# Kernel tuning notes

Hardware: AMD Instinct MI355X
Metric: run time of the kernel (lower is better)

The kernel has to match this reference:

```python
import jax, jax.numpy as jnp
import numpy as np

N, E, G, M = 65536, 262144, 1024, 64   # nodes, edges, graphs, max nodes/graph
D, H, C, ED, P, L = 512, 8, 64, 128, 1024, 5  # hidden, heads, head_dim, edge_dim, proj_dim, layers
SLOPE = 0.2  # PyG GATv2 leaky_relu negative slope


def rmsnorm(x, w):
    eps = jnp.asarray(jnp.finfo(x.dtype).eps, x.dtype)
    return x * jax.lax.rsqrt(jnp.mean(x * x, axis=-1, keepdims=True) + eps) * w


def gat_layer(x, src, dst, eattr, Wl, bl, Wr, br, We, att, gb):
    # GATv2Conv(concat=True, edge_dim, add_self_loops=False), eval mode
    xl = (x @ Wl + bl).reshape(N, H, C)
    xr = (x @ Wr + br).reshape(N, H, C)
    ee = (eattr @ We).reshape(E, H, C)
    s = xl[src] + xr[dst] + ee                      # [E,H,C]
    s = jnp.where(s > 0, s, SLOPE * s)              # leaky_relu
    logits = jnp.einsum('ehc,hc->eh', s, att)       # [E,H]
    mx = jax.ops.segment_max(logits, dst, num_segments=N)
    p = jnp.exp(logits - mx[dst])
    denom = jax.ops.segment_sum(p, dst, num_segments=N)
    alpha = p / denom[dst]                          # segment softmax over in-edges of dst
    msg = xl[src] * alpha[:, :, None]               # [E,H,C]
    return jax.ops.segment_sum(msg, dst, num_segments=N).reshape(N, H * C) + gb


def setup_inputs():
    key = jax.random.key(0)
    ks = jax.random.split(key, 32)
    f = lambda k, shp: 0.02 * jax.random.normal(k, shp, dtype=jnp.float32)
    inp = {}
    inp['node_x'] = jax.random.randint(ks[0], (N, 9), 0, 2, dtype=jnp.int32)
    inp['edge_attr_idx'] = jax.random.randint(ks[1], (E, 3), 0, 2, dtype=jnp.int32)
    inp['edge_index'] = jax.random.randint(ks[2], (2, E), 0, N, dtype=jnp.int32)
    inp['batch'] = jnp.arange(N, dtype=jnp.int32) // M  # sorted graph ids, 64 atoms/graph
    # MolEncoder embedding tables, padded to max vocab (indices stay in-range)
    inp['atom_emb'] = f(ks[3], (9, 119, D))
    inp['edge_emb'] = f(ks[4], (3, 22, ED))
    # 5 GATv2Block layers, params stacked on leading axis
    inp['Wl'] = f(ks[5], (L, D, D)); inp['bl'] = f(ks[6], (L, D))
    inp['Wr'] = f(ks[7], (L, D, D)); inp['br'] = f(ks[8], (L, D))
    inp['We'] = f(ks[9], (L, ED, D))
    inp['att'] = f(ks[10], (L, H, C))
    inp['gb'] = f(ks[11], (L, D))
    inp['n1w'] = jnp.ones((L, D), jnp.float32)
    inp['f1w'] = f(ks[12], (L, D, 4 * D)); inp['f1b'] = f(ks[13], (L, 4 * D))
    inp['f2w'] = f(ks[14], (L, 4 * D, D)); inp['f2b'] = f(ks[15], (L, D))
    inp['n2w'] = jnp.ones((L, D), jnp.float32)
    # attention pooling + projection head
    inp['gapW'] = f(ks[16], (D, D)); inp['gapb'] = f(ks[17], (D,))
    inp['avW'] = f(ks[18], (D,)); inp['avb'] = f(ks[19], (1,))
    inp['p1W'] = f(ks[20], (D, P)); inp['p1b'] = f(ks[21], (P,))
    inp['pnw'] = jnp.ones((P,), jnp.float32)
    inp['p2W'] = f(ks[22], (P, P)); inp['p2b'] = f(ks[23], (P,))
    return inp


def reference(node_x, edge_attr_idx, edge_index, batch, atom_emb, edge_emb, Wl, bl, Wr, br, We, att, gb, n1w, f1w, f1b, f2w, f2b, n2w, gapW, gapb, avW, avb, p1W, p1b, pnw, p2W, p2b):
    src, dst = edge_index[0], edge_index[1]
    # MolEncoder: sum of categorical embeddings
    x = atom_emb[jnp.arange(9)[None, :], node_x].sum(axis=1)              # [N,D]
    eattr = edge_emb[jnp.arange(3)[None, :], edge_attr_idx].sum(axis=1)   # [E,ED]
    for l in range(L):
        xa = gat_layer(x, src, dst, eattr, Wl[l], bl[l], Wr[l], br[l], We[l], att[l], gb[l])
        x = rmsnorm(x + xa, n1w[l])
        h = jax.nn.gelu(x @ f1w[l] + f1b[l], approximate=False) @ f2w[l] + f2b[l]
        x = rmsnorm(x + h, n2w[l])
    # to_dense_batch with static max_nodes = M
    counts = jax.ops.segment_sum(jnp.ones(N, jnp.int32), batch, num_segments=G)
    starts = jnp.concatenate([jnp.zeros(1, jnp.int32), jnp.cumsum(counts)[:-1].astype(jnp.int32)])
    pos = jnp.arange(N, dtype=jnp.int32) - starts[batch]
    x_dense = jnp.zeros((G, M, D), x.dtype).at[batch, pos].set(x)
    mask = jnp.zeros((G, M), bool).at[batch, pos].set(True)
    # graph attention pooling
    z = x_dense @ gapW + gapb                                             # [G,M,D]
    a = (z @ avW + avb[0])[:, :, None]                                    # [G,M,1]
    a = jnp.where(mask[:, :, None], a, -jnp.inf)
    alpha = jax.nn.softmax(a, axis=1)
    h_graph = jnp.sum(z * alpha, axis=1)                                  # [G,D]
    hp = jax.nn.relu(rmsnorm(h_graph @ p1W + p1b, pnw))
    z_graph_pool = hp @ p2W + p2b                                         # [G,P]
    return z_graph_pool, x_dense, mask
```

## Files before the change

### kernel.cpp

```cpp
#include <hip/hip_runtime.h>
#include <hip/hip_bf16.h>
#include <math.h>

namespace {

using bf16 = __hip_bfloat16;
typedef __bf16 bf16x8 __attribute__((ext_vector_type(8)));
typedef float f32x4 __attribute__((ext_vector_type(4)));

constexpr int N_ = 65536, E_ = 262144, G_ = 1024, M_ = 64;
constexpr int D_ = 512, H_ = 8, C_ = 64, ED_ = 128, P_ = 1024, L_ = 5;
constexpr float SLOPE = 0.2f;
constexpr float EPSF = 1.1920929e-7f;

constexpr int NCH = 2;
constexpr int NCHUNK = N_ / NCH;

constexpr int TV = 22;
constexpr int TK = TV * TV * TV;
constexpr int TKP = 10752;

constexpr int CH = 4;

__device__ inline float b2f(bf16 h) { return __bfloat162float(h); }
__device__ inline bf16 f2b(float f) { return __float2bfloat16(f); }
__device__ inline float us2f(unsigned short u) {
  return __uint_as_float((unsigned)u << 16);
}
__device__ inline unsigned short f2us(float f) {
  bf16 b = __float2bfloat16(f);
  return *(unsigned short*)&b;
}

typedef __attribute__((address_space(1))) void as1_void_t;
typedef __attribute__((address_space(3))) void as3_void_t;
__device__ inline void gload16(const void* g, void* l) {
  __builtin_amdgcn_global_load_lds((const as1_void_t*)g, (as3_void_t*)l, 16, 0,
                                   0);
}

template <int EPI, int OBF>
__global__ __launch_bounds__(256) void mfma_gemm_k(
    const ushort* __restrict__ A, const ushort* __restrict__ Bt,
    const float* __restrict__ bias, void* __restrict__ Cv, int M, int K,
    int Nc) {
  __shared__ __align__(16) ushort As[128 * 64];
  __shared__ __align__(16) ushort Bs[128 * 64];
  const int tid = threadIdx.x;
  const int wave = tid >> 6, lane = tid & 63;
  const int m0 = blockIdx.x * 128, n0 = blockIdx.y * 128;
  const int wr = wave >> 1, wc = wave & 1;
  const int srow = tid >> 3;
  const int skoff = (((tid & 7) ^ (srow & 7)) << 3);
  const ushort* Ap = A + (size_t)(m0 + srow) * K + skoff;
  const ushort* Bp = Bt + (size_t)(n0 + srow) * K + skoff;
  char* AsB = (char*)As + wave * 1024;
  char* BsB = (char*)Bs + wave * 1024;
  const int fr = lane & 15, fg = lane >> 4;
  const int rx = fr & 7;
  const int sA0 = ((fg) ^ rx) << 3;
  const int sA1 = ((4 | fg) ^ rx) << 3;
  const ushort* Arow = As + (wr * 64 + fr) * 64;
  const ushort* Brow = Bs + (wc * 64 + fr) * 64;
  f32x4 acc[4][4];
#pragma unroll
  for (int i = 0; i < 4; ++i)
#pragma unroll
    for (int j = 0; j < 4; ++j) acc[i][j] = (f32x4){0.f, 0.f, 0.f, 0.f};

  for (int kt = 0; kt < K; kt += 64) {
#pragma unroll
    for (int r = 0; r < 4; ++r) {
      gload16(Ap + kt + (size_t)r * 32 * K, AsB + r * 4096);
      gload16(Bp + kt + (size_t)r * 32 * K, BsB + r * 4096);
    }
    __syncthreads();
    bf16x8 af[4], bg[4];
#pragma unroll
    for (int i = 0; i < 4; ++i)
      af[i] = *(const bf16x8*)(Arow + i * 1024 + sA0);
#pragma unroll
    for (int j = 0; j < 4; ++j)
      bg[j] = *(const bf16x8*)(Brow + j * 1024 + sA0);
#pragma unroll
    for (int i = 0; i < 4; ++i)
#pragma unroll
      for (int j = 0; j < 4; ++j)
        acc[i][j] = __builtin_amdgcn_mfma_f32_16x16x32_bf16(af[i], bg[j],
                                                            acc[i][j], 0, 0, 0);
#pragma unroll
    for (int i = 0; i < 4; ++i)
      af[i] = *(const bf16x8*)(Arow + i * 1024 + sA1);
#pragma unroll
    for (int j = 0; j < 4; ++j)
      bg[j] = *(const bf16x8*)(Brow + j * 1024 + sA1);
#pragma unroll
    for (int i = 0; i < 4; ++i)
#pragma unroll
      for (int j = 0; j < 4; ++j)
        acc[i][j] = __builtin_amdgcn_mfma_f32_16x16x32_bf16(af[i], bg[j],
                                                            acc[i][j], 0, 0, 0);
    __syncthreads();
  }
  const int cb = n0 + wc * 64 + fr;
  float bv[4];
#pragma unroll
  for (int j = 0; j < 4; ++j) bv[j] = bias ? bias[cb + j * 16] : 0.f;
#pragma unroll
  for (int i = 0; i < 4; ++i) {
#pragma unroll
    for (int r = 0; r < 4; ++r) {
      int m = m0 + wr * 64 + i * 16 + fg * 4 + r;
      size_t rb = (size_t)m * Nc + cb;
#pragma unroll
      for (int j = 0; j < 4; ++j) {
        float c = acc[i][j][r] + bv[j];
        if (EPI == 1) c = 0.5f * c * (1.f + erff(c * 0.70710678118654752f));
        if (OBF)
          ((bf16*)Cv)[rb + j * 16] = f2b(c);
        else
          ((float*)Cv)[rb + j * 16] = c;
      }
    }
  }
}

__global__ __launch_bounds__(256) void transpose_cvt_k(
    const float* __restrict__ W, bf16* __restrict__ Wt, int K, int N) {
  __shared__ float tile[32][33];
  int bn = blockIdx.x * 32, bk = blockIdx.y * 32;
  int tx = threadIdx.x, ty = threadIdx.y;
#pragma unroll
  for (int i = ty; i < 32; i += 8) tile[i][tx] = W[(size_t)(bk + i) * N + bn + tx];
  __syncthreads();
#pragma unroll
  for (int i = ty; i < 32; i += 8)
    Wt[(size_t)(bn + i) * K + bk + tx] = f2b(tile[tx][i]);
}

template <int EPI, typename TIN, typename TOUT>
__global__ __launch_bounds__(256) void gemm_bias_k(
    const TIN* __restrict__ A, const float* __restrict__ B,
    const float* __restrict__ bias, TOUT* __restrict__ C, int M, int K,
    int Nc) {
  __shared__ float As[64][17];
  __shared__ float Bs[16][68];
  const int tid = threadIdx.x;
  const int m0 = blockIdx.x * 64;
  const int n0 = blockIdx.y * 64;
  const int ty = tid >> 4, tx = tid & 15;
  const int lam = tid >> 2;
  const int lak = (tid & 3) << 2;
  const int lbk = tid >> 4;
  const int lbn = (tid & 15) << 2;
  const TIN* Aptr = A + (long)(m0 + lam) * K + lak;
  const float* Bptr = B + (long)lbk * Nc + n0 + lbn;
  float acc[4][4] = {};
  for (int kt = 0; kt < K; kt += 16) {
    float4 va = *(const float4*)(Aptr + kt);
    float4 vb = *(const float4*)(Bptr + (long)kt * Nc);
    __syncthreads();
    As[lam][lak + 0] = va.x; As[lam][lak + 1] = va.y;
    As[lam][lak + 2] = va.z; As[lam][lak + 3] = va.w;
    Bs[lbk][lbn + 0] = vb.x; Bs[lbk][lbn + 1] = vb.y;
    Bs[lbk][lbn + 2] = vb.z; Bs[lbk][lbn + 3] = vb.w;
    __syncthreads();
#pragma unroll
    for (int kk = 0; kk < 16; ++kk) {
      float a[4], b[4];
#pragma unroll
      for (int i = 0; i < 4; ++i) a[i] = As[ty * 4 + i][kk];
#pragma unroll
      for (int j = 0; j < 4; ++j) b[j] = Bs[kk][tx * 4 + j];
#pragma unroll
      for (int i = 0; i < 4; ++i)
#pragma unroll
        for (int j = 0; j < 4; ++j) acc[i][j] = fmaf(a[i], b[j], acc[i][j]);
    }
  }
#pragma unroll
  for (int i = 0; i < 4; ++i) {
    long row = (long)(m0 + ty * 4 + i) * Nc + n0;
#pragma unroll
    for (int j = 0; j < 4; ++j) {
      float c = acc[i][j] + (bias ? bias[n0 + tx * 4 + j] : 0.f);
      if (EPI == 1) c = 0.5f * c * (1.f + erff(c * 0.70710678118654752f));
      ((float*)C)[row + tx * 4 + j] = c;
    }
  }
}

__global__ __launch_bounds__(256) void encode_nodes_k(
    const int* __restrict__ nodeX, const float* __restrict__ atomEmb,
    bf16* __restrict__ x) {
  int n = blockIdx.x, tid = threadIdx.x;
  __shared__ int idx[9];
  if (tid < 9) idx[tid] = nodeX[n * 9 + tid];
  __syncthreads();
  for (int d = tid; d < D_; d += 256) {
    float s = 0.f;
#pragma unroll
    for (int k = 0; k < 9; ++k) s += atomEmb[(k * 119 + idx[k]) * D_ + d];
    x[(long)n * D_ + d] = f2b(s);
  }
}

__global__ __launch_bounds__(256) void build_keys_k(
    const int* __restrict__ eai, int* __restrict__ keys) {
  int e = blockIdx.x * 256 + threadIdx.x;
  keys[e] = eai[e * 3] * (TV * TV) + eai[e * 3 + 1] * TV + eai[e * 3 + 2];
}

__global__ __launch_bounds__(128) void build_eattr_tab_k(
    const float* __restrict__ edgeEmb, bf16* __restrict__ tab) {
  int r = blockIdx.x, d = threadIdx.x;
  float s = 0.f;
  if (r < TK) {
    int k0 = r / (TV * TV), k1 = (r / TV) % TV, k2 = r % TV;
    s = edgeEmb[(0 * TV + k0) * ED_ + d] + edgeEmb[(1 * TV + k1) * ED_ + d] +
        edgeEmb[(2 * TV + k2) * ED_ + d];
  }
  tab[(size_t)r * ED_ + d] = f2b(s);
}

__global__ __launch_bounds__(256) void gat_fused_k(
    bf16* __restrict__ x, const ushort* __restrict__ xl,
    const ushort* __restrict__ xr, const ushort* __restrict__ ee_tab,
    const int* __restrict__ keys, const float* __restrict__ att,
    const int* __restrict__ ptr, const int* __restrict__ eid,
    const int* __restrict__ src, const float* __restrict__ gb,
    const float* __restrict__ w) {
  const int wave = threadIdx.x >> 6, lane = threadIdx.x & 63;
  const int n = blockIdx.x * 4 + wave;
  const int d0 = lane * 8;
  const int beg = ptr[n], deg = ptr[n + 1] - beg;

  float4 a0 = *(const float4*)(att + d0);
  float4 a1 = *(const float4*)(att + d0 + 4);
  float attv[8] = {a0.x, a0.y, a0.z, a0.w, a1.x, a1.y, a1.z, a1.w};
  uint4 xru = *(const uint4*)(xr + (size_t)n * D_ + d0);
  float xrf[8];
#pragma unroll
  for (int q = 0; q < 4; ++q) {
    unsigned u = (&xru.x)[q];
    xrf[2 * q] = us2f((ushort)u);
    xrf[2 * q + 1] = us2f((ushort)(u >> 16));
  }

  float m = -__builtin_inff(), den = 0.f;
  float acc[8] = {0.f, 0.f, 0.f, 0.f, 0.f, 0.f, 0.f, 0.f};

  for (int c0 = 0; c0 < deg; c0 += CH) {
    int cn = min(deg - c0, CH);
    int s_l = 0, k_l = 0;
    if (lane < cn) {
      int e = eid[beg + c0 + lane];
      s_l = src[e];
      k_l = keys[e];
    }
    uint4 xlv[CH];
    float lg[CH];
#pragma unroll
    for (int i = 0; i < CH; ++i) {
      lg[i] = -__builtin_inff();
      if (i < cn) {
        int s = __shfl(s_l, i);
        int k = __shfl(k_l, i);
        xlv[i] = *(const uint4*)(xl + (size_t)s * D_ + d0);
        uint4 ev = *(const uint4*)(ee_tab + (size_t)k * D_ + d0);
        float part = 0.f;
#pragma unroll
        for (int q = 0; q < 4; ++q) {
          unsigned ua = (&xlv[i].x)[q];
          unsigned ue = (&ev.x)[q];
          float v0 = us2f((ushort)ua) + xrf[2 * q] + us2f((ushort)ue);
          float v1 =
              us2f((ushort)(ua >> 16)) + xrf[2 * q + 1] + us2f((ushort)(ue >> 16));
          v0 = (v0 > 0.f) ? v0 : SLOPE * v0;
          v1 = (v1 > 0.f) ? v1 : SLOPE * v1;
          part = fmaf(v0, attv[2 * q], part);
          part = fmaf(v1, attv[2 * q + 1], part);
        }
        part += __shfl_xor(part, 1);
        part += __shfl_xor(part, 2);
        part += __shfl_xor(part, 4);
        lg[i] = part;
      }
    }
    float cm = lg[0];
#pragma unroll
    for (int i = 1; i < CH; ++i) cm = fmaxf(cm, lg[i]);
    if (cm > m) {
      float sc = expf(m - cm);
      den *= sc;
#pragma unroll
      for (int j = 0; j < 8; ++j) acc[j] *= sc;
      m = cm;
    }
#pragma unroll
    for (int i = 0; i < CH; ++i) {
      if (i < cn) {
        float p = expf(lg[i] - m);
        den += p;
#pragma unroll
        for (int q = 0; q < 4; ++q) {
          unsigned ua = (&xlv[i].x)[q];
          acc[2 * q] = fmaf(us2f((ushort)ua), p, acc[2 * q]);
          acc[2 * q + 1] = fmaf(us2f((ushort)(ua >> 16)), p, acc[2 * q + 1]);
        }
      }
    }
  }

  float inv = (deg > 0) ? 1.f / den : 0.f;
  uint4 xu = *(const uint4*)((const ushort*)x + (size_t)n * D_ + d0);
  float4 g0 = *(const float4*)(gb + d0);
  float4 g1 = *(const float4*)(gb + d0 + 4);
  float gbv[8] = {g0.x, g0.y, g0.z, g0.w, g1.x, g1.y, g1.z, g1.w};
  float v[8], ss = 0.f;
#pragma unroll
  for (int q = 0; q < 4; ++q) {
    unsigned u = (&xu.x)[q];
    v[2 * q] = us2f((ushort)u) + acc[2 * q] * inv + gbv[2 * q];
    v[2 * q + 1] = us2f((ushort)(u >> 16)) + acc[2 * q + 1] * inv + gbv[2 * q + 1];
  }
#pragma unroll
  for (int j = 0; j < 8; ++j) ss += v[j] * v[j];
#pragma unroll
  for (int o = 1; o < 64; o <<= 1) ss += __shfl_xor(ss, o);
  float scale = rsqrtf(ss * (1.0f / D_) + EPSF);
  float4 w0 = *(const float4*)(w + d0);
  float4 w1 = *(const float4*)(w + d0 + 4);
  float wv[8] = {w0.x, w0.y, w0.z, w0.w, w1.x, w1.y, w1.z, w1.w};
  uint4 outv;
#pragma unroll
  for (int q = 0; q < 4; ++q) {
    unsigned lo = f2us(v[2 * q] * scale * wv[2 * q]);
    unsigned hi = f2us(v[2 * q + 1] * scale * wv[2 * q + 1]);
    (&outv.x)[q] = lo | (hi << 16);
  }
  *(uint4*)((ushort*)x + (size_t)n * D_ + d0) = outv;
}

__global__ __launch_bounds__(256) void rmsnorm_res_k(
    bf16* __restrict__ x, const float* __restrict__ xa,
    const float* __restrict__ w) {
  int n = blockIdx.x, tid = threadIdx.x;
  long base = (long)n * D_;
  float v0 = b2f(x[base + tid]) + xa[base + tid];
  float v1 = b2f(x[base + tid + 256]) + xa[base + tid + 256];
  float ss = v0 * v0 + v1 * v1;
#pragma unroll
  for (int o = 32; o > 0; o >>= 1) ss += __shfl_xor(ss, o);
  __shared__ float wsum[4];
  if ((tid & 63) == 0) wsum[tid >> 6] = ss;
  __syncthreads();
  float tot = wsum[0] + wsum[1] + wsum[2] + wsum[3];
  float scale = rsqrtf(tot * (1.0f / D_) + EPSF);
  x[base + tid] = f2b(v0 * scale * w[tid]);
  x[base + tid + 256] = f2b(v1 * scale * w[tid + 256]);
}

__global__ void zero_int_k(int* __restrict__ p) {
  p[blockIdx.x * 256 + threadIdx.x] = 0;
}
__global__ void count_k(const int* __restrict__ key, int* __restrict__ counts) {
  int id = blockIdx.x * 256 + threadIdx.x;
  atomicAdd(&counts[key[id]], 1);
}
__global__ void copy_int_k(const int* __restrict__ in, int* __restrict__ out) {
  int id = blockIdx.x * 256 + threadIdx.x;
  out[id] = in[id];
}
__global__ void fill_csr_k(const int* __restrict__ dst,
                           int* __restrict__ cursor, int* __restrict__ eid) {
  int e = blockIdx.x * 256 + threadIdx.x;
  int pos = atomicAdd(&cursor[dst[e]], 1);
  eid[pos] = e;
}
__global__ __launch_bounds__(1024) void scanN_k(const int* __restrict__ cnt,
                                                int* __restrict__ ptr) {
  __shared__ int sums[1024];
  int t = threadIdx.x;
  int base = t * 64;
  int s = 0;
  for (int i = 0; i < 64; ++i) s += cnt[base + i];
  sums[t] = s;
  __syncthreads();
  for (int off = 1; off < 1024; off <<= 1) {
    int v = (t >= off) ? sums[t - off] : 0;
    __syncthreads();
    sums[t] += v;
    __syncthreads();
  }
  int run = (t > 0) ? sums[t - 1] : 0;
  for (int i = 0; i < 64; ++i) {
    ptr[base + i] = run;
    run += cnt[base + i];
  }
  if (t == 1023) ptr[N_] = run;
}
__global__ void scan_k(const int* __restrict__ counts, int* __restrict__ starts) {
  __shared__ int buf[G_];
  int t = threadIdx.x;
  int c = counts[t];
  buf[t] = c;
  __syncthreads();
  for (int off = 1; off < G_; off <<= 1) {
    int v = (t >= off) ? buf[t - off] : 0;
    __syncthreads();
    buf[t] += v;
    __syncthreads();
  }
  starts[t] = buf[t] - c;
}

__global__ __launch_bounds__(256) void pool_k(
    const bf16* __restrict__ z, const float* __restrict__ avW,
    const float* __restrict__ avb, const int* __restrict__ counts,
    const int* __restrict__ starts, float* __restrict__ hg) {
  int g = blockIdx.x, tid = threadIdx.x;
  int cnt = counts[g], st = starts[g];
  __shared__ float aL[M_];
  int wave = tid >> 6, lane = tid & 63;
  for (int m = wave; m < M_; m += 4) {
    float s = 0.f;
    if (m < cnt) {
      const bf16* row = z + (long)(st + m) * D_;
      for (int c = lane; c < D_; c += 64) s += b2f(row[c]) * avW[c];
    }
#pragma unroll
    for (int o = 32; o > 0; o >>= 1) s += __shfl_xor(s, o);
    if (lane == 0) aL[m] = s;
  }
  __syncthreads();
  if (tid < 64) {
    float v = (tid < cnt) ? aL[tid] + avb[0] : -__builtin_inff();
    float mxv = v;
#pragma unroll
    for (int o = 32; o > 0; o >>= 1) mxv = fmaxf(mxv, __shfl_xor(mxv, o));
    float p = (tid < cnt) ? expf(v - mxv) : 0.f;
    float sm = p;
#pragma unroll
    for (int o = 32; o > 0; o >>= 1) sm += __shfl_xor(sm, o);
    aL[tid] = p / sm;
  }
  __syncthreads();
  for (int d = tid; d < D_; d += 256) {
    float acc = 0.f;
    for (int m = 0; m < cnt; ++m) acc += b2f(z[(long)(st + m) * D_ + d]) * aL[m];
    hg[(long)g * D_ + d] = acc;
  }
}

__global__ __launch_bounds__(256) void rms_relu_k(
    const float* __restrict__ in, const float* __restrict__ w,
    float* __restrict__ out) {
  int g = blockIdx.x, tid = threadIdx.x;
  long base = (long)g * P_;
  float v[4], ss = 0.f;
#pragma unroll
  for (int k = 0; k < 4; ++k) {
    v[k] = in[base + tid + k * 256];
    ss += v[k] * v[k];
  }
#pragma unroll
  for (int o = 32; o > 0; o >>= 1) ss += __shfl_xor(ss, o);
  __shared__ float wsum[4];
  if ((tid & 63) == 0) wsum[tid >> 6] = ss;
  __syncthreads();
  float tot = wsum[0] + wsum[1] + wsum[2] + wsum[3];
  float scale = rsqrtf(tot * (1.0f / P_) + EPSF);
#pragma unroll
  for (int k = 0; k < 4; ++k) {
    float c = v[k] * scale * w[tid + k * 256];
    out[base + tid + k * 256] = fmaxf(c, 0.f);
  }
}

__global__ __launch_bounds__(256) void write_dense_k(
    const bf16* __restrict__ x, const int* __restrict__ counts,
    const int* __restrict__ starts, float* __restrict__ out1) {
  long id = (long)blockIdx.x * 256 + threadIdx.x;
  int g = (int)(id >> 15);
  int rem = (int)(id & 32767);
  int m = rem >> 9, d = rem & 511;
  float v = 0.f;
  if (m < counts[g]) v = b2f(x[(long)(starts[g] + m) * D_ + d]);
  out1[id] = v;
}
__global__ void write_mask_k(const int* __restrict__ counts,
                             float* __restrict__ out2) {
  int id = blockIdx.x * 256 + threadIdx.x;
  out2[id] = ((id & 63) < counts[id >> 6]) ? 1.f : 0.f;
}

}

extern "C" void kernel_launch(void* const* d_in, const int* in_sizes, int n_in,
                              void* d_out, int out_size, void* d_ws,
                              size_t ws_size, hipStream_t stream) {
  const int* node_x = (const int*)d_in[0];
  const int* edge_attr_idx = (const int*)d_in[1];
  const int* edge_index = (const int*)d_in[2];
  const int* batch = (const int*)d_in[3];
  const float* atom_emb = (const float*)d_in[4];
  const float* edge_emb = (const float*)d_in[5];
  const float* Wl = (const float*)d_in[6];
  const float* bl = (const float*)d_in[7];
  const float* Wr = (const float*)d_in[8];
  const float* br = (const float*)d_in[9];
  const float* We = (const float*)d_in[10];
  const float* att = (const float*)d_in[11];
  const float* gb = (const float*)d_in[12];
  const float* n1w = (const float*)d_in[13];
  const float* f1w = (const float*)d_in[14];
  const float* f1b = (const float*)d_in[15];
  const float* f2w = (const float*)d_in[16];
  const float* f2b = (const float*)d_in[17];
  const float* n2w = (const float*)d_in[18];
  const float* gapW = (const float*)d_in[19];
  const float* gapb = (const float*)d_in[20];
  const float* avW = (const float*)d_in[21];
  const float* avb = (const float*)d_in[22];
  const float* p1W = (const float*)d_in[23];
  const float* p1b = (const float*)d_in[24];
  const float* pnw = (const float*)d_in[25];
  const float* p2W = (const float*)d_in[26];
  const float* p2b = (const float*)d_in[27];
  const int* src = edge_index;
  const int* dst = edge_index + E_;

  char* ws = (char*)d_ws;
  bf16* x = (bf16*)ws;
  bf16* xl = x + (long)N_ * D_;
  bf16* xr = xl + (long)N_ * D_;
  bf16* region = xr + (long)N_ * D_;
  bf16* ee_tab = region;
  bf16* eattr_tab = ee_tab + (long)TKP * D_;
  float* logits_unused = (float*)(region + (long)32768 * D_ + (long)32768 * ED_);
  int* keys = (int*)(logits_unused + (long)E_ * H_);
  float* denom_unused = (float*)(keys + N_ * H_);
  int* counts = (int*)(denom_unused + (long)N_ * H_);
  int* starts = counts + G_;
  float* hg = (float*)(starts + G_);
  float* tmpP = hg + (long)G_ * D_;
  float* hp = tmpP + (long)G_ * P_;
  bf16* hid = xl;

  bf16* wsc = (bf16*)tmpP;
  bf16* Wl_b = wsc;
  bf16* Wr_b = Wl_b + 512 * 512;
  bf16* We_b = Wr_b + 512 * 512;
  bf16* f1w_b = We_b + 512 * 128;
  bf16* f2w_b = f1w_b + 2048 * 512;

  float* out0 = (float*)d_out;
  float* out1 = out0 + (long)G_ * P_;
  float* out2 = out1 + (long)G_ * M_ * D_;
  float* xa = out1;

  int* csr_eid = (int*)out0;
  int* csr_ptr = csr_eid + E_;
  int* cursor = csr_ptr + N_ + 1;

  encode_nodes_k<<<N_, 256, 0, stream>>>(node_x, atom_emb, x);

  build_keys_k<<<E_ / 256, 256, 0, stream>>>(edge_attr_idx, keys);
  build_eattr_tab_k<<<TKP, 128, 0, stream>>>(edge_emb, eattr_tab);
  zero_int_k<<<N_ / 256, 256, 0, stream>>>(cursor);
  count_k<<<E_ / 256, 256, 0, stream>>>(dst, cursor);
  scanN_k<<<1, 1024, 0, stream>>>(cursor, csr_ptr);
  copy_int_k<<<N_ / 256, 256, 0, stream>>>(csr_ptr, cursor);
  fill_csr_k<<<E_ / 256, 256, 0, stream>>>(dst, cursor, csr_eid);

  for (int l = 0; l < L_; ++l) {
    const float* Wl_l = Wl + (long)l * D_ * D_;
    const float* bl_l = bl + (long)l * D_;
    const float* Wr_l = Wr + (long)l * D_ * D_;
    const float* br_l = br + (long)l * D_;
    const float* We_l = We + (long)l * ED_ * D_;
    const float* att_l = att + (long)l * H_ * C_;
    const float* gb_l = gb + (long)l * D_;
    const float* n1w_l = n1w + (long)l * D_;
    const float* f1w_l = f1w + (long)l * D_ * 4 * D_;
    const float* f1b_l = f1b + (long)l * 4 * D_;
    const float* f2w_l = f2w + (long)l * 4 * D_ * D_;
    const float* f2b_l = f2b + (long)l * D_;
    const float* n2w_l = n2w + (long)l * D_;

    transpose_cvt_k<<<dim3(16, 16), dim3(32, 8), 0, stream>>>(Wl_l, Wl_b, 512, 512);
    transpose_cvt_k<<<dim3(16, 16), dim3(32, 8), 0, stream>>>(Wr_l, Wr_b, 512, 512);
    transpose_cvt_k<<<dim3(16, 4), dim3(32, 8), 0, stream>>>(We_l, We_b, 128, 512);
    transpose_cvt_k<<<dim3(64, 16), dim3(32, 8), 0, stream>>>(f1w_l, f1w_b, 512, 2048);
    transpose_cvt_k<<<dim3(16, 64), dim3(32, 8), 0, stream>>>(f2w_l, f2w_b, 2048, 512);

    mfma_gemm_k<0, 1><<<dim3(N_ / 128, D_ / 128), 256, 0, stream>>>(
        (const ushort*)x, (const ushort*)Wl_b, bl_l, xl, N_, D_, D_);
    mfma_gemm_k<0, 1><<<dim3(N_ / 128, D_ / 128), 256, 0, stream>>>(
        (const ushort*)x, (const ushort*)Wr_b, br_l, xr, N_, D_, D_);
    mfma_gemm_k<0, 1><<<dim3(TKP / 128, D_ / 128), 256, 0, stream>>>(
        (const ushort*)eattr_tab, (const ushort*)We_b, nullptr, ee_tab, TKP,
        ED_, D_);

    gat_fused_k<<<N_ / 4, 256, 0, stream>>>(
        x, (const ushort*)xl, (const ushort*)xr, (const ushort*)ee_tab, keys,
        att_l, csr_ptr, csr_eid, src, gb_l, n1w_l);

    for (int nc = 0; nc < NCH; ++nc) {
      long nbase = (long)nc * NCHUNK;
      mfma_gemm_k<1, 1><<<dim3(NCHUNK / 128, (4 * D_) / 128), 256, 0, stream>>>(
          (const ushort*)(x + nbase * D_), (const ushort*)f1w_b, f1b_l, hid,
          NCHUNK, D_, 4 * D_);
      mfma_gemm_k<0, 0><<<dim3(NCHUNK / 128, D_ / 128), 256, 0, stream>>>(
          (const ushort*)hid, (const ushort*)f2w_b, f2b_l, xa + nbase * D_,
          NCHUNK, 4 * D_, D_);
    }
    rmsnorm_res_k<<<N_, 256, 0, stream>>>(x, xa, n2w_l);
  }

  zero_int_k<<<G_ / 256, 256, 0, stream>>>(counts);
  count_k<<<N_ / 256, 256, 0, stream>>>(batch, counts);
  scan_k<<<1, G_, 0, stream>>>(counts, starts);

  bf16* gapW_b = eattr_tab;
  transpose_cvt_k<<<dim3(16, 16), dim3(32, 8), 0, stream>>>(gapW, gapW_b, 512, 512);
  mfma_gemm_k<0, 1><<<dim3(N_ / 128, D_ / 128), 256, 0, stream>>>(
      (const ushort*)x, (const ushort*)gapW_b, gapb, xl, N_, D_, D_);
  pool_k<<<G_, 256, 0, stream>>>(xl, avW, avb, counts, starts, hg);
  gemm_bias_k<0, float, float><<<dim3(G_ / 64, P_ / 64), 256, 0, stream>>>(
      hg, p1W, p1b, tmpP, G_, D_, P_);
  rms_relu_k<<<G_, 256, 0, stream>>>(tmpP, pnw, hp);
  gemm_bias_k<0, float, float><<<dim3(G_ / 64, P_ / 64), 256, 0, stream>>>(
      hp, p2W, p2b, out0, G_, P_, P_);

  write_dense_k<<<(int)(((long)G_ * M_ * D_) / 256), 256, 0, stream>>>(
      x, counts, starts, out1);
  write_mask_k<<<(G_ * M_) / 256, 256, 0, stream>>>(counts, out2);
}
```

Before: 4.118 ms.

## Double-buffer MFMA GEMM LDS, fuse Wl/Wr GEMMs, batch weight prep, fast GELU

The MFMA GEMM now uses two LDS buffers, so the next K tile's global-to-LDS loads are issued before the current tile is computed, which hides load latency and removes one barrier per iteration. The Wl and Wr projections are merged into a single N=1024 GEMM writing an interleaved xlr buffer, and the GAT kernel reads from it. The five per-layer weight transposes are merged into one prep kernel that also concatenates the two biases. erff in the GELU epilogue is replaced by an Abramowitz-Stegun polynomial approximation, which slightly changes numerics. Double buffering doubles LDS use to 64KB per block, which may lower occupancy.

```diff
diff --git a/kernel.cpp b/kernel.cpp
--- a/kernel.cpp
+++ b/kernel.cpp
@@ -30,6 +30,20 @@
 __device__ inline unsigned short f2us(float f) {
   bf16 b = __float2bfloat16(f);
   return *(unsigned short*)&b;
+}
+
+__device__ inline float fast_gelu(float c) {
+  float z = c * 0.70710678118654752f;
+  float az = fabsf(z);
+  float t = __builtin_amdgcn_rcpf(1.f + 0.3275911f * az);
+  float e = __expf(-az * az);
+  float poly =
+      t * (0.254829592f +
+           t * (-0.284496736f +
+                t * (1.421413741f + t * (-1.453152027f + t * 1.061405429f))));
+  float r = 1.f - poly * e;
+  float erfv = (z < 0.f) ? -r : r;
+  return 0.5f * c * (1.f + erfv);
 }
 
 typedef __attribute__((address_space(1))) void as1_void_t;
@@ -44,8 +58,8 @@
     const ushort* __restrict__ A, const ushort* __restrict__ Bt,
     const float* __restrict__ bias, void* __restrict__ Cv, int M, int K,
     int Nc) {
-  __shared__ __align__(16) ushort As[128 * 64];
-  __shared__ __align__(16) ushort Bs[128 * 64];
+  __shared__ __align__(16) ushort As[2][128 * 64];
+  __shared__ __align__(16) ushort Bs[2][128 * 64];
   const int tid = threadIdx.x;
   const int wave = tid >> 6, lane = tid & 63;
   const int m0 = blockIdx.x * 128, n0 = blockIdx.y * 128;
@@ -54,34 +68,33 @@
   const int skoff = (((tid & 7) ^ (srow & 7)) << 3);
   const ushort* Ap = A + (size_t)(m0 + srow) * K + skoff;
   const ushort* Bp = Bt + (size_t)(n0 + srow) * K + skoff;
-  char* AsB = (char*)As + wave * 1024;
-  char* BsB = (char*)Bs + wave * 1024;
   const int fr = lane & 15, fg = lane >> 4;
   const int rx = fr & 7;
   const int sA0 = ((fg) ^ rx) << 3;
   const int sA1 = ((4 | fg) ^ rx) << 3;
-  const ushort* Arow = As + (wr * 64 + fr) * 64;
-  const ushort* Brow = Bs + (wc * 64 + fr) * 64;
   f32x4 acc[4][4];
 #pragma unroll
   for (int i = 0; i < 4; ++i)
 #pragma unroll
     for (int j = 0; j < 4; ++j) acc[i][j] = (f32x4){0.f, 0.f, 0.f, 0.f};
 
-  for (int kt = 0; kt < K; kt += 64) {
+  auto STAGE = [&](int buf, int kt) {
 #pragma unroll
     for (int r = 0; r < 4; ++r) {
-      gload16(Ap + kt + (size_t)r * 32 * K, AsB + r * 4096);
-      gload16(Bp + kt + (size_t)r * 32 * K, BsB + r * 4096);
-    }
-    __syncthreads();
+      gload16(Ap + kt + (size_t)r * 32 * K,
+              (char*)As[buf] + wave * 1024 + r * 4096);
+      gload16(Bp + kt + (size_t)r * 32 * K,
+              (char*)Bs[buf] + wave * 1024 + r * 4096);
+    }
+  };
+  auto COMPUTE = [&](int buf) {
+    const ushort* Arow = As[buf] + (wr * 64 + fr) * 64;
+    const ushort* Brow = Bs[buf] + (wc * 64 + fr) * 64;
     bf16x8 af[4], bg[4];
 #pragma unroll
-    for (int i = 0; i < 4; ++i)
-      af[i] = *(const bf16x8*)(Arow + i * 1024 + sA0);
-#pragma unroll
-    for (int j = 0; j < 4; ++j)
-      bg[j] = *(const bf16x8*)(Brow + j * 1024 + sA0);
+    for (int i = 0; i < 4; ++i) af[i] = *(const bf16x8*)(Arow + i * 1024 + sA0);
+#pragma unroll
+    for (int j = 0; j < 4; ++j) bg[j] = *(const bf16x8*)(Brow + j * 1024 + sA0);
 #pragma unroll
     for (int i = 0; i < 4; ++i)
 #pragma unroll
@@ -89,19 +102,28 @@
         acc[i][j] = __builtin_amdgcn_mfma_f32_16x16x32_bf16(af[i], bg[j],
                                                             acc[i][j], 0, 0, 0);
 #pragma unroll
-    for (int i = 0; i < 4; ++i)
-      af[i] = *(const bf16x8*)(Arow + i * 1024 + sA1);
-#pragma unroll
-    for (int j = 0; j < 4; ++j)
-      bg[j] = *(const bf16x8*)(Brow + j * 1024 + sA1);
+    for (int i = 0; i < 4; ++i) af[i] = *(const bf16x8*)(Arow + i * 1024 + sA1);
+#pragma unroll
+    for (int j = 0; j < 4; ++j) bg[j] = *(const bf16x8*)(Brow + j * 1024 + sA1);
 #pragma unroll
     for (int i = 0; i < 4; ++i)
 #pragma unroll
       for (int j = 0; j < 4; ++j)
         acc[i][j] = __builtin_amdgcn_mfma_f32_16x16x32_bf16(af[i], bg[j],
                                                             acc[i][j], 0, 0, 0);
+  };
+
+  STAGE(0, 0);
+  __syncthreads();
+  int cur = 0;
+  for (int kt = 64; kt < K; kt += 64) {
+    STAGE(cur ^ 1, kt);
+    COMPUTE(cur);
     __syncthreads();
-  }
+    cur ^= 1;
+  }
+  COMPUTE(cur);
+
   const int cb = n0 + wc * 64 + fr;
   float bv[4];
 #pragma unroll
@@ -115,7 +137,7 @@
 #pragma unroll
       for (int j = 0; j < 4; ++j) {
         float c = acc[i][j][r] + bv[j];
-        if (EPI == 1) c = 0.5f * c * (1.f + erff(c * 0.70710678118654752f));
+        if (EPI == 1) c = fast_gelu(c);
         if (OBF)
           ((bf16*)Cv)[rb + j * 16] = f2b(c);
         else
@@ -125,17 +147,56 @@
   }
 }
 
+__device__ inline void tr_tile(const float* __restrict__ W,
+                               bf16* __restrict__ Wt, int K, int N,
+                               int tileIdx, float* tile ) {
+  int tilesN = N >> 5;
+  int bn = (tileIdx % tilesN) << 5, bk = (tileIdx / tilesN) << 5;
+  int tx = threadIdx.x & 31, ty = threadIdx.x >> 5;
+#pragma unroll
+  for (int i = ty; i < 32; i += 8)
+    tile[i * 33 + tx] = W[(size_t)(bk + i) * N + bn + tx];
+  __syncthreads();
+#pragma unroll
+  for (int i = ty; i < 32; i += 8)
+    Wt[(size_t)(bn + i) * K + bk + tx] = f2b(tile[tx * 33 + i]);
+}
+
+__global__ __launch_bounds__(256) void prep_weights_k(
+    const float* __restrict__ Wl, const float* __restrict__ Wr,
+    const float* __restrict__ We, const float* __restrict__ f1w,
+    const float* __restrict__ f2w, const float* __restrict__ bl,
+    const float* __restrict__ br, bf16* __restrict__ Wlr_b,
+    bf16* __restrict__ We_b, bf16* __restrict__ f1w_b,
+    bf16* __restrict__ f2w_b, float* __restrict__ blr) {
+  __shared__ float tile[32 * 33];
+  int bid = blockIdx.x;
+  if (bid < 256) {
+    tr_tile(Wl, Wlr_b, 512, 512, bid, tile);
+  } else if (bid < 512) {
+    tr_tile(Wr, Wlr_b + 512 * 512, 512, 512, bid - 256, tile);
+  } else if (bid < 576) {
+    tr_tile(We, We_b, 128, 512, bid - 512, tile);
+  } else if (bid < 1600) {
+    tr_tile(f1w, f1w_b, 512, 2048, bid - 576, tile);
+  } else if (bid < 2624) {
+    tr_tile(f2w, f2w_b, 2048, 512, bid - 1600, tile);
+  } else {
+    int t = threadIdx.x;
+#pragma unroll
+    for (int k = 0; k < 4; ++k) {
+      int i = t + k * 256;
+      blr[i] = (i < 512) ? bl[i] : br[i - 512];
+    }
+  }
+}
+
 __global__ __launch_bounds__(256) void transpose_cvt_k(
     const float* __restrict__ W, bf16* __restrict__ Wt, int K, int N) {
-  __shared__ float tile[32][33];
-  int bn = blockIdx.x * 32, bk = blockIdx.y * 32;
-  int tx = threadIdx.x, ty = threadIdx.y;
-#pragma unroll
-  for (int i = ty; i < 32; i += 8) tile[i][tx] = W[(size_t)(bk + i) * N + bn + tx];
-  __syncthreads();
-#pragma unroll
-  for (int i = ty; i < 32; i += 8)
-    Wt[(size_t)(bn + i) * K + bk + tx] = f2b(tile[tx][i]);
+  __shared__ float tile[32 * 33];
+  int tilesN = N >> 5;
+  tr_tile(W, Wt, K, N, blockIdx.x + blockIdx.y * tilesN * 0, tile);
+  (void)tilesN;
 }
 
 template <int EPI, typename TIN, typename TOUT>
@@ -184,7 +245,7 @@
 #pragma unroll
     for (int j = 0; j < 4; ++j) {
       float c = acc[i][j] + (bias ? bias[n0 + tx * 4 + j] : 0.f);
-      if (EPI == 1) c = 0.5f * c * (1.f + erff(c * 0.70710678118654752f));
+      if (EPI == 1) c = fast_gelu(c);
       ((float*)C)[row + tx * 4 + j] = c;
     }
   }
@@ -224,12 +285,11 @@
 }
 
 __global__ __launch_bounds__(256) void gat_fused_k(
-    bf16* __restrict__ x, const ushort* __restrict__ xl,
-    const ushort* __restrict__ xr, const ushort* __restrict__ ee_tab,
-    const int* __restrict__ keys, const float* __restrict__ att,
-    const int* __restrict__ ptr, const int* __restrict__ eid,
-    const int* __restrict__ src, const float* __restrict__ gb,
-    const float* __restrict__ w) {
+    bf16* __restrict__ x, const ushort* __restrict__ xlr,
+    const ushort* __restrict__ ee_tab, const int* __restrict__ keys,
+    const float* __restrict__ att, const int* __restrict__ ptr,
+    const int* __restrict__ eid, const int* __restrict__ src,
+    const float* __restrict__ gb, const float* __restrict__ w) {
   const int wave = threadIdx.x >> 6, lane = threadIdx.x & 63;
   const int n = blockIdx.x * 4 + wave;
   const int d0 = lane * 8;
@@ -238,7 +298,7 @@
   float4 a0 = *(const float4*)(att + d0);
   float4 a1 = *(const float4*)(att + d0 + 4);
   float attv[8] = {a0.x, a0.y, a0.z, a0.w, a1.x, a1.y, a1.z, a1.w};
-  uint4 xru = *(const uint4*)(xr + (size_t)n * D_ + d0);
+  uint4 xru = *(const uint4*)(xlr + (size_t)n * 1024 + 512 + d0);
   float xrf[8];
 #pragma unroll
   for (int q = 0; q < 4; ++q) {
@@ -266,7 +326,7 @@
       if (i < cn) {
         int s = __shfl(s_l, i);
         int k = __shfl(k_l, i);
-        xlv[i] = *(const uint4*)(xl + (size_t)s * D_ + d0);
+        xlv[i] = *(const uint4*)(xlr + (size_t)s * 1024 + d0);
         uint4 ev = *(const uint4*)(ee_tab + (size_t)k * D_ + d0);
         float part = 0.f;
 #pragma unroll
@@ -533,27 +593,26 @@
 
   char* ws = (char*)d_ws;
   bf16* x = (bf16*)ws;
-  bf16* xl = x + (long)N_ * D_;
-  bf16* xr = xl + (long)N_ * D_;
-  bf16* region = xr + (long)N_ * D_;
+  bf16* xlr = x + (long)N_ * D_;
+  bf16* region = xlr + (long)N_ * 1024;
   bf16* ee_tab = region;
   bf16* eattr_tab = ee_tab + (long)TKP * D_;
-  float* logits_unused = (float*)(region + (long)32768 * D_ + (long)32768 * ED_);
-  int* keys = (int*)(logits_unused + (long)E_ * H_);
-  float* denom_unused = (float*)(keys + N_ * H_);
-  int* counts = (int*)(denom_unused + (long)N_ * H_);
+  float* spare = (float*)(region + (long)32768 * D_ + (long)32768 * ED_);
+  int* keys = (int*)(spare + (long)E_ * H_);
+  float* spare2 = (float*)(keys + N_ * H_);
+  int* counts = (int*)(spare2 + (long)N_ * H_);
   int* starts = counts + G_;
   float* hg = (float*)(starts + G_);
   float* tmpP = hg + (long)G_ * D_;
   float* hp = tmpP + (long)G_ * P_;
-  bf16* hid = xl;
+  bf16* hid = xlr;
 
   bf16* wsc = (bf16*)tmpP;
-  bf16* Wl_b = wsc;
-  bf16* Wr_b = Wl_b + 512 * 512;
-  bf16* We_b = Wr_b + 512 * 512;
+  bf16* Wlr_b = wsc;
+  bf16* We_b = Wlr_b + 1024 * 512;
   bf16* f1w_b = We_b + 512 * 128;
   bf16* f2w_b = f1w_b + 2048 * 512;
+  float* blr = (float*)(f2w_b + 512 * 2048);
 
   float* out0 = (float*)d_out;
   float* out1 = out0 + (long)G_ * P_;
@@ -589,23 +648,19 @@
     const float* f2b_l = f2b + (long)l * D_;
     const float* n2w_l = n2w + (long)l * D_;
 
-    transpose_cvt_k<<<dim3(16, 16), dim3(32, 8), 0, stream>>>(Wl_l, Wl_b, 512, 512);
-    transpose_cvt_k<<<dim3(16, 16), dim3(32, 8), 0, stream>>>(Wr_l, Wr_b, 512, 512);
-    transpose_cvt_k<<<dim3(16, 4), dim3(32, 8), 0, stream>>>(We_l, We_b, 128, 512);
-    transpose_cvt_k<<<dim3(64, 16), dim3(32, 8), 0, stream>>>(f1w_l, f1w_b, 512, 2048);
-    transpose_cvt_k<<<dim3(16, 64), dim3(32, 8), 0, stream>>>(f2w_l, f2w_b, 2048, 512);
-
-    mfma_gemm_k<0, 1><<<dim3(N_ / 128, D_ / 128), 256, 0, stream>>>(
-        (const ushort*)x, (const ushort*)Wl_b, bl_l, xl, N_, D_, D_);
-    mfma_gemm_k<0, 1><<<dim3(N_ / 128, D_ / 128), 256, 0, stream>>>(
-        (const ushort*)x, (const ushort*)Wr_b, br_l, xr, N_, D_, D_);
+    prep_weights_k<<<2625, 256, 0, stream>>>(Wl_l, Wr_l, We_l, f1w_l, f2w_l,
+                                             bl_l, br_l, Wlr_b, We_b, f1w_b,
+                                             f2w_b, blr);
+
+    mfma_gemm_k<0, 1><<<dim3(N_ / 128, 1024 / 128), 256, 0, stream>>>(
+        (const ushort*)x, (const ushort*)Wlr_b, blr, xlr, N_, D_, 1024);
     mfma_gemm_k<0, 1><<<dim3(TKP / 128, D_ / 128), 256, 0, stream>>>(
         (const ushort*)eattr_tab, (const ushort*)We_b, nullptr, ee_tab, TKP,
         ED_, D_);
 
     gat_fused_k<<<N_ / 4, 256, 0, stream>>>(
-        x, (const ushort*)xl, (const ushort*)xr, (const ushort*)ee_tab, keys,
-        att_l, csr_ptr, csr_eid, src, gb_l, n1w_l);
+        x, (const ushort*)xlr, (const ushort*)ee_tab, keys, att_l, csr_ptr,
+        csr_eid, src, gb_l, n1w_l);
 
     for (int nc = 0; nc < NCH; ++nc) {
       long nbase = (long)nc * NCHUNK;
@@ -624,10 +679,11 @@
   scan_k<<<1, G_, 0, stream>>>(counts, starts);
 
   bf16* gapW_b = eattr_tab;
-  transpose_cvt_k<<<dim3(16, 16), dim3(32, 8), 0, stream>>>(gapW, gapW_b, 512, 512);
+  transpose_cvt_k<<<256, 256, 0, stream>>>(gapW, gapW_b, 512, 512);
+  bf16* z = xlr;
   mfma_gemm_k<0, 1><<<dim3(N_ / 128, D_ / 128), 256, 0, stream>>>(
-      (const ushort*)x, (const ushort*)gapW_b, gapb, xl, N_, D_, D_);
-  pool_k<<<G_, 256, 0, stream>>>(xl, avW, avb, counts, starts, hg);
+      (const ushort*)x, (const ushort*)gapW_b, gapb, z, N_, D_, D_);
+  pool_k<<<G_, 256, 0, stream>>>(z, avW, avb, counts, starts, hg);
   gemm_bias_k<0, float, float><<<dim3(G_ / 64, P_ / 64), 256, 0, stream>>>(
       hg, p1W, p1b, tmpP, G_, D_, P_);
   rms_relu_k<<<G_, 256, 0, stream>>>(tmpP, pnw, hp);
```

Result: no change. 4.141 ms (+0.6%).
